# Kernel optimization log

Measured on AMD Instinct MI355X. Metric: run time of the kernel, lower is better.

The kernel has to match this reference:

```python
import jax, jax.numpy as jnp
import numpy as np

D_MODEL, D_INNER, D_STATE, DT_RANK, K = 768, 1536, 16, 48, 4
B, L = 2, 1024


def causal_depthwise_conv(x, w, b):
    # x: [B, L, D], w: [D, 1, K], b: [D]; torch pads K-1 both sides then slices [:L] -> causal left pad
    xt = x.transpose(0, 2, 1)  # [B, D, L]
    out = jax.lax.conv_general_dilated(
        xt, w, window_strides=(1,), padding=[(K - 1, 0)],
        dimension_numbers=('NCH', 'OIH', 'NCH'), feature_group_count=xt.shape[1])
    return out.transpose(0, 2, 1) + b


def ssm(xc, A_log, D, W_dt, dtW, dtb, W_B, W_C):
    # xc: [B, L, Din]
    A = -jnp.exp(A_log)                                   # [Din, N]
    dt_low = jnp.einsum('bld,rd->blr', xc, W_dt)          # [B, L, R]
    delta = jax.nn.softplus(jnp.einsum('blr,dr->bld', dt_low, dtW) + dtb)  # [B, L, Din]
    Bm = jnp.einsum('bld,nd->bln', xc, W_B)               # [B, L, N]
    Cm = jnp.einsum('bld,nd->bln', xc, W_C)               # [B, L, N]
    deltaA = jnp.exp(delta[..., None] * A)                # [B, L, Din, N]
    BX = (delta * xc)[..., None] * Bm[:, :, None, :]      # [B, L, Din, N]

    def combine(e1, e2):
        a1, b1 = e1
        a2, b2 = e2
        return a1 * a2, a2 * b1 + b2

    _, hs = jax.lax.associative_scan(combine, (deltaA, BX), axis=1)  # [B, L, Din, N]
    y = jnp.einsum('bldn,bln->bld', hs, Cm) + D * xc
    return y


def setup_inputs() -> dict:
    key = jax.random.key(0)
    ks = jax.random.split(key, 20)
    s = 0.02
    A_init = jnp.log(jnp.broadcast_to(jnp.arange(1, D_STATE + 1, dtype=jnp.float32), (D_INNER, D_STATE)))
    return {
        'x': jax.random.normal(ks[0], (B, L, D_MODEL), jnp.float32),
        'W_in_states': jax.random.normal(ks[1], (D_INNER, D_MODEL), jnp.float32) * s,
        'W_in_gates': jax.random.normal(ks[2], (D_INNER, D_MODEL), jnp.float32) * s,
        'conv_w': jax.random.normal(ks[3], (D_INNER, 1, K), jnp.float32) * 0.2,
        'conv_b': jax.random.normal(ks[4], (D_INNER,), jnp.float32) * 0.02,
        'conv_w_b': jax.random.normal(ks[5], (D_INNER, 1, K), jnp.float32) * 0.2,
        'conv_b_b': jax.random.normal(ks[6], (D_INNER,), jnp.float32) * 0.02,
        'W_dt': jax.random.normal(ks[7], (DT_RANK, D_INNER), jnp.float32) * s,
        'W_B': jax.random.normal(ks[8], (D_STATE, D_INNER), jnp.float32) * s,
        'W_C': jax.random.normal(ks[9], (D_STATE, D_INNER), jnp.float32) * s,
        'dtW': jax.random.normal(ks[10], (D_INNER, DT_RANK), jnp.float32) * s,
        'dtb': jax.random.normal(ks[11], (D_INNER,), jnp.float32) * 0.1,
        'A_log': A_init,
        'Dp': jnp.ones((D_INNER,), jnp.float32),
        'W_dt_b': jax.random.normal(ks[12], (DT_RANK, D_INNER), jnp.float32) * s,
        'W_B_b': jax.random.normal(ks[13], (D_STATE, D_INNER), jnp.float32) * s,
        'W_C_b': jax.random.normal(ks[14], (D_STATE, D_INNER), jnp.float32) * s,
        'dtW_b': jax.random.normal(ks[15], (D_INNER, DT_RANK), jnp.float32) * s,
        'dtb_b': jax.random.normal(ks[16], (D_INNER,), jnp.float32) * 0.1,
        'A_log_b': A_init,
        'Dp_b': jnp.ones((D_INNER,), jnp.float32),
        'W_out': jax.random.normal(ks[17], (D_MODEL, D_INNER), jnp.float32) * s,
    }


def reference(x, W_in_states, W_in_gates, conv_w, conv_b, conv_w_b, conv_b_b,
              W_dt, W_B, W_C, dtW, dtb, A_log, Dp,
              W_dt_b, W_B_b, W_C_b, dtW_b, dtb_b, A_log_b, Dp_b, W_out):
    xs = jnp.einsum('blm,dm->bld', x, W_in_states)  # [B, L, Din]
    z = jnp.einsum('blm,dm->bld', x, W_in_gates)    # [B, L, Din]
    # forward branch
    xc = jax.nn.silu(causal_depthwise_conv(xs, conv_w, conv_b))
    y = ssm(xc, A_log, Dp, W_dt, dtW, dtb, W_B, W_C)
    # backward branch: xz flipped along L, split -> reversed xs / reversed z
    xs_b = xs[:, ::-1]
    z_b = z[:, ::-1]
    xcb = jax.nn.silu(causal_depthwise_conv(xs_b, conv_w_b, conv_b_b))
    y_b = ssm(xcb, A_log_b, Dp_b, W_dt_b, dtW_b, dtb_b, W_B_b, W_C_b)
    # gating
    y = y * jax.nn.silu(z)
    y_b = y_b * jax.nn.silu(z_b)
    y = (y + y_b[:, ::-1]) * 0.5  # divide_output
    return jnp.einsum('bld,md->blm', y, W_out)
```

## Files before the change

kernel.cpp:

```cpp
#include <hip/hip_runtime.h>
#include <hip/hip_bf16.h>
#include <stdint.h>

#define DM 768
#define DI 1536
#define DSTATE 16
#define RNK 48
#define BB 2
#define LL 1024
#define ML (BB * LL)

#define NSEG 32
#define SEGL (LL / NSEG)

#define PROJ_NCHUNK 8
#define PROJ_KC (DI / PROJ_NCHUNK)

typedef unsigned short u16;
typedef __bf16 bf16x8 __attribute__((ext_vector_type(8)));
typedef float f32x4 __attribute__((ext_vector_type(4)));

struct __align__(8) u16x4_t { u16 x, y, z, w; };

__device__ __forceinline__ float b2f(u16 u) {
  union { uint32_t i; float f; } v; v.i = ((uint32_t)u) << 16; return v.f;
}
__device__ __forceinline__ u16 f2b(float f) {
  union { float f; uint32_t i; } v; v.f = f;
  uint32_t r = v.i + 0x7FFFu + ((v.i >> 16) & 1u);
  return (u16)(r >> 16);
}
__device__ __forceinline__ float silu_f(float x) { return x / (1.f + __expf(-x)); }
__device__ __forceinline__ float softplus_f(float s) {
  return fmaxf(s, 0.f) + __logf(1.f + __expf(-fabsf(s)));
}
__device__ __forceinline__ u16x4_t cvt4(float4 v) {
  u16x4_t o; o.x = f2b(v.x); o.y = f2b(v.y); o.z = f2b(v.z); o.w = f2b(v.w); return o;
}

__device__ __forceinline__ void gl16(const u16* g, u16* l) {
  __builtin_amdgcn_global_load_lds(
      (const __attribute__((address_space(1))) uint32_t*)g,
      (__attribute__((address_space(3))) uint32_t*)l, 16, 0, 0);
}

#define SEG_X    (ML * DM / 4)
#define SEG_W    (DI * DM / 4)
#define SEG_CAT  (128 * DI / 4)
#define SEG_DTW  (DI * 64 / 4)
__global__ __launch_bounds__(256) void convert_kernel(
    const float4* __restrict__ x, const float4* __restrict__ wis,
    const float4* __restrict__ wig, const float4* __restrict__ wout,
    const float* __restrict__ W_B, const float* __restrict__ W_C,
    const float* __restrict__ W_dt,
    const float* __restrict__ W_B_b, const float* __restrict__ W_C_b,
    const float* __restrict__ W_dt_b,
    const float* __restrict__ dtW, const float* __restrict__ dtW_b,
    u16x4_t* __restrict__ xb, u16x4_t* __restrict__ wisb,
    u16x4_t* __restrict__ wigb, u16x4_t* __restrict__ woutb,
    u16x4_t* __restrict__ wcf, u16x4_t* __restrict__ wcb,
    u16x4_t* __restrict__ dtwf, u16x4_t* __restrict__ dtwb)
{
  int idx = blockIdx.x * 256 + threadIdx.x;
  if (idx < SEG_X) { xb[idx] = cvt4(x[idx]); return; }
  idx -= SEG_X;
  if (idx < SEG_W) { wisb[idx] = cvt4(wis[idx]); return; }
  idx -= SEG_W;
  if (idx < SEG_W) { wigb[idx] = cvt4(wig[idx]); return; }
  idx -= SEG_W;
  if (idx < SEG_W) { woutb[idx] = cvt4(wout[idx]); return; }
  idx -= SEG_W;
  if (idx < 2 * SEG_CAT) {
    int dir = idx / SEG_CAT;
    int rem = idx % SEG_CAT;
    int row = rem / (DI / 4), k4 = rem % (DI / 4);
    const float* src = nullptr;
    if (row < 16)      src = (dir ? W_B_b  : W_B)  + (size_t)row * DI + k4 * 4;
    else if (row < 32) src = (dir ? W_C_b  : W_C)  + (size_t)(row - 16) * DI + k4 * 4;
    else if (row < 80) src = (dir ? W_dt_b : W_dt) + (size_t)(row - 32) * DI + k4 * 4;
    u16x4_t o;
    if (src) o = cvt4(*(const float4*)src);
    else { o.x = 0; o.y = 0; o.z = 0; o.w = 0; }
    (dir ? wcb : wcf)[rem] = o;
    return;
  }
  idx -= 2 * SEG_CAT;
  int dir = idx / SEG_DTW;
  int rem = idx % SEG_DTW;
  int d = rem / 16, r4 = rem % 16;
  const float* Dw = dir ? dtW_b : dtW;
  u16x4_t o;
  if (r4 < 12) o = cvt4(*(const float4*)(Dw + (size_t)d * RNK + r4 * 4));
  else { o.x = 0; o.y = 0; o.z = 0; o.w = 0; }
  (dir ? dtwb : dtwf)[rem] = o;
}

__global__ __launch_bounds__(256) void gemm_bt(
    const u16* __restrict__ A, const u16* __restrict__ B0,
    const u16* __restrict__ B1, int Nsplit,
    void* __restrict__ Cout, int M, int N, int K, int ldc, int epi,
    const u16* __restrict__ A2, const u16* __restrict__ B2,
    void* __restrict__ C2,
    const float* __restrict__ ebias, const float* __restrict__ ebias2)
{
  if (blockIdx.z) { A = A2; B0 = B2; Cout = C2; ebias = ebias2; }
  __shared__ alignas(16) u16 As[2][128 * 32];
  __shared__ alignas(16) u16 Bs[2][128 * 32];
  const int tid = threadIdx.x;
  const int wave = tid >> 6, lane = tid & 63;
  const int bm = blockIdx.y * 128;
  const int bn = blockIdx.x * 128;

  const u16* Bmat = B0;
  int ncol0 = bn;
  int epi_l = epi;
  if (B1 != nullptr && bn >= Nsplit) { Bmat = B1; ncol0 = bn - Nsplit; epi_l = 1; }

  const int c0 = tid, c1 = tid + 256;
  const u16* gA0 = A + (size_t)(bm + (c0 >> 2)) * K + (c0 & 3) * 8;
  const u16* gA1 = A + (size_t)(bm + (c1 >> 2)) * K + (c1 & 3) * 8;
  const u16* gB0 = Bmat + (size_t)(ncol0 + (c0 >> 2)) * K + (c0 & 3) * 8;
  const u16* gB1 = Bmat + (size_t)(ncol0 + (c1 >> 2)) * K + (c1 & 3) * 8;

  const int wm = (wave & 1) * 64, wn = (wave >> 1) * 64;
  const int rl = lane & 15, q = lane >> 4;

  f32x4 acc[4][4];
#pragma unroll
  for (int i = 0; i < 4; ++i)
#pragma unroll
    for (int j = 0; j < 4; ++j) acc[i][j] = (f32x4){0.f, 0.f, 0.f, 0.f};

  auto stage = [&](int buf, int k0) {
    gl16(gA0 + k0, &As[buf][c0 * 8]);
    gl16(gA1 + k0, &As[buf][c1 * 8]);
    gl16(gB0 + k0, &Bs[buf][c0 * 8]);
    gl16(gB1 + k0, &Bs[buf][c1 * 8]);
  };

  stage(0, 0);
  __syncthreads();
  int cur = 0;
  for (int k0 = 0; k0 < K; k0 += 32) {
    const bool more = (k0 + 32 < K);
    if (more) stage(cur ^ 1, k0 + 32);

    const bf16x8* AsV = (const bf16x8*)As[cur];
    const bf16x8* BsV = (const bf16x8*)Bs[cur];
    bf16x8 af[4], bfv[4];
#pragma unroll
    for (int s = 0; s < 4; ++s) {
      af[s]  = AsV[(wm + s * 16 + rl) * 4 + q];
      bfv[s] = BsV[(wn + s * 16 + rl) * 4 + q];
    }
#pragma unroll
    for (int i = 0; i < 4; ++i)
#pragma unroll
      for (int j = 0; j < 4; ++j)
        acc[i][j] = __builtin_amdgcn_mfma_f32_16x16x32_bf16(af[i], bfv[j], acc[i][j], 0, 0, 0);

    if (more) {
      __syncthreads();
      cur ^= 1;
    }
  }

#pragma unroll
  for (int i = 0; i < 4; ++i) {
#pragma unroll
    for (int j = 0; j < 4; ++j) {
#pragma unroll
      for (int r = 0; r < 4; ++r) {
        int row = bm + wm + i * 16 + q * 4 + r;
        int col = bn + wn + j * 16 + rl;
        float v = acc[i][j][r];
        if (epi_l == 1) v = silu_f(v);
        if (epi == 6) {
          ((u16*)Cout)[(size_t)row * ldc + col] = f2b(softplus_f(v + ebias[col]));
        } else {
          ((u16*)Cout)[(size_t)row * ldc + col] = f2b(v);
        }
      }
    }
  }
}

__global__ __launch_bounds__(256) void gemm_proj_sk(
    const u16* __restrict__ xcf, const u16* __restrict__ xcb,
    const u16* __restrict__ wcf, const u16* __restrict__ wcb,
    float* __restrict__ part)
{
  const int dir = blockIdx.z;
  const u16* A = dir ? xcb : xcf;
  const u16* B = dir ? wcb : wcf;
  const int kc = blockIdx.x;
  const int bm = blockIdx.y * 128;
  const int kbase = kc * PROJ_KC;

  __shared__ alignas(16) u16 As[128 * 32];
  __shared__ alignas(16) u16 Bs[128 * 32];
  const int tid = threadIdx.x;
  const int wave = tid >> 6, lane = tid & 63;
  const int c0 = tid, c1 = tid + 256;
  const u16* gA0 = A + (size_t)(bm + (c0 >> 2)) * DI + kbase + (c0 & 3) * 8;
  const u16* gA1 = A + (size_t)(bm + (c1 >> 2)) * DI + kbase + (c1 & 3) * 8;
  const u16* gB0 = B + (size_t)(c0 >> 2) * DI + kbase + (c0 & 3) * 8;
  const u16* gB1 = B + (size_t)(c1 >> 2) * DI + kbase + (c1 & 3) * 8;
  uint4* lA0 = (uint4*)&As[c0 * 8]; uint4* lA1 = (uint4*)&As[c1 * 8];
  uint4* lB0 = (uint4*)&Bs[c0 * 8]; uint4* lB1 = (uint4*)&Bs[c1 * 8];

  const int wm = (wave & 1) * 64, wn = (wave >> 1) * 64;
  const int rl = lane & 15, q = lane >> 4;

  f32x4 acc[4][4];
#pragma unroll
  for (int i = 0; i < 4; ++i)
#pragma unroll
    for (int j = 0; j < 4; ++j) acc[i][j] = (f32x4){0.f, 0.f, 0.f, 0.f};

  const bf16x8* AsV = (const bf16x8*)As;
  const bf16x8* BsV = (const bf16x8*)Bs;

  uint4 ra0 = *(const uint4*)(gA0);
  uint4 ra1 = *(const uint4*)(gA1);
  uint4 rb0 = *(const uint4*)(gB0);
  uint4 rb1 = *(const uint4*)(gB1);

  for (int k0 = 0; k0 < PROJ_KC; k0 += 32) {
    *lA0 = ra0; *lA1 = ra1; *lB0 = rb0; *lB1 = rb1;
    __syncthreads();
    if (k0 + 32 < PROJ_KC) {
      ra0 = *(const uint4*)(gA0 + k0 + 32);
      ra1 = *(const uint4*)(gA1 + k0 + 32);
      rb0 = *(const uint4*)(gB0 + k0 + 32);
      rb1 = *(const uint4*)(gB1 + k0 + 32);
    }
    bf16x8 af[4], bfv[4];
#pragma unroll
    for (int s = 0; s < 4; ++s) {
      af[s]  = AsV[(wm + s * 16 + rl) * 4 + q];
      bfv[s] = BsV[(wn + s * 16 + rl) * 4 + q];
    }
#pragma unroll
    for (int i = 0; i < 4; ++i)
#pragma unroll
      for (int j = 0; j < 4; ++j)
        acc[i][j] = __builtin_amdgcn_mfma_f32_16x16x32_bf16(af[i], bfv[j], acc[i][j], 0, 0, 0);
    __syncthreads();
  }

  float* pout = part + ((size_t)(dir * PROJ_NCHUNK + kc) * ML + bm) * 128;
#pragma unroll
  for (int i = 0; i < 4; ++i) {
#pragma unroll
    for (int j = 0; j < 4; ++j) {
#pragma unroll
      for (int r = 0; r < 4; ++r) {
        int row = wm + i * 16 + q * 4 + r;
        int col = wn + j * 16 + rl;
        if (col < 96)
          pout[(size_t)row * 128 + col] = acc[i][j][r];
      }
    }
  }
}

__global__ __launch_bounds__(256) void proj_reduce(
    const float* __restrict__ part,
    float* __restrict__ pf, float* __restrict__ pb,
    u16* __restrict__ dtlf, u16* __restrict__ dtlb)
{
  int idx = blockIdx.x * 256 + threadIdx.x;
  int col = idx % 96;
  int t = idx / 96;
  int row = t % ML;
  int dir = t / ML;
  const float* p = part + ((size_t)dir * PROJ_NCHUNK * ML + row) * 128 + col;
  float s = 0.f;
#pragma unroll
  for (int c = 0; c < PROJ_NCHUNK; ++c)
    s += p[(size_t)c * ML * 128];
  if (col < 32) (dir ? pb : pf)[(size_t)row * 32 + col] = s;
  else          (dir ? dtlb : dtlf)[(size_t)row * 64 + (col - 32)] = f2b(s);
}

__global__ __launch_bounds__(256) void gemm_out64(
    const u16* __restrict__ A, const u16* __restrict__ Bw,
    float* __restrict__ out)
{
  __shared__ alignas(16) u16 As[64 * 72];
  __shared__ alignas(16) u16 Bs[64 * 72];
  const int tid = threadIdx.x;
  const int wave = tid >> 6, lane = tid & 63;
  const int bm = blockIdx.y * 64;
  const int bn = blockIdx.x * 64;

  const int c0 = tid, c1 = tid + 256;
  const u16* gA0 = A + (size_t)(bm + (c0 >> 3)) * DI + (c0 & 7) * 8;
  const u16* gA1 = A + (size_t)(bm + (c1 >> 3)) * DI + (c1 & 7) * 8;
  const u16* gB0 = Bw + (size_t)(bn + (c0 >> 3)) * DI + (c0 & 7) * 8;
  const u16* gB1 = Bw + (size_t)(bn + (c1 >> 3)) * DI + (c1 & 7) * 8;
  uint4* lA0 = (uint4*)&As[(c0 >> 3) * 72 + (c0 & 7) * 8];
  uint4* lA1 = (uint4*)&As[(c1 >> 3) * 72 + (c1 & 7) * 8];
  uint4* lB0 = (uint4*)&Bs[(c0 >> 3) * 72 + (c0 & 7) * 8];
  uint4* lB1 = (uint4*)&Bs[(c1 >> 3) * 72 + (c1 & 7) * 8];

  const int rl = lane & 15, q = lane >> 4;

  f32x4 acc[4];
#pragma unroll
  for (int s = 0; s < 4; ++s) acc[s] = (f32x4){0.f, 0.f, 0.f, 0.f};

  uint4 ra0 = *(const uint4*)gA0, ra1 = *(const uint4*)gA1;
  uint4 rb0 = *(const uint4*)gB0, rb1 = *(const uint4*)gB1;

  for (int k0 = 0; k0 < DI; k0 += 64) {
    *lA0 = ra0; *lA1 = ra1; *lB0 = rb0; *lB1 = rb1;
    __syncthreads();
    if (k0 + 64 < DI) {
      ra0 = *(const uint4*)(gA0 + k0 + 64);
      ra1 = *(const uint4*)(gA1 + k0 + 64);
      rb0 = *(const uint4*)(gB0 + k0 + 64);
      rb1 = *(const uint4*)(gB1 + k0 + 64);
    }
    bf16x8 bf[2], af;
#pragma unroll
    for (int c = 0; c < 2; ++c)
      bf[c] = *(const bf16x8*)&Bs[(wave * 16 + rl) * 72 + c * 32 + q * 8];
#pragma unroll
    for (int s = 0; s < 4; ++s) {
#pragma unroll
      for (int c = 0; c < 2; ++c) {
        af = *(const bf16x8*)&As[(s * 16 + rl) * 72 + c * 32 + q * 8];
        acc[s] = __builtin_amdgcn_mfma_f32_16x16x32_bf16(af, bf[c], acc[s], 0, 0, 0);
      }
    }
    __syncthreads();
  }

#pragma unroll
  for (int s = 0; s < 4; ++s) {
#pragma unroll
    for (int r = 0; r < 4; ++r) {
      int row = bm + s * 16 + q * 4 + r;
      int col = bn + wave * 16 + rl;
      out[(size_t)row * DM + col] = acc[s][r];
    }
  }
}

__global__ void conv_kernel(
    const u16* __restrict__ xsg,
    const float* __restrict__ cw, const float* __restrict__ cb,
    const float* __restrict__ cwb, const float* __restrict__ cbb,
    u16* __restrict__ xc, u16* __restrict__ xcb)
{
  int idx = blockIdx.x * 256 + threadIdx.x;
  int d = idx % DI;
  int row = idx / DI;
  int l = row % LL, b = row / LL;
  const u16* base = xsg + (size_t)b * LL * 3072 + d;

  float4 wf = *(const float4*)(cw + d * 4);
  float4 wb = *(const float4*)(cwb + d * 4);
  float wfk[4] = {wf.x, wf.y, wf.z, wf.w};
  float wbk[4] = {wb.x, wb.y, wb.z, wb.w};

  float accf = cb[d];
  float accb = cbb[d];
#pragma unroll
  for (int k = 0; k < 4; ++k) {
    int ls = l - 3 + k;
    if (ls >= 0) {
      accf += wfk[k] * b2f(base[(size_t)ls * 3072]);
      accb += wbk[k] * b2f(base[(size_t)(LL - 1 - ls) * 3072]);
    }
  }
  xc[idx]  = f2b(silu_f(accf));
  xcb[idx] = f2b(silu_f(accb));
}

__global__ __launch_bounds__(256) void scan_sum(
    const u16* __restrict__ df, const u16* __restrict__ db,
    const u16* __restrict__ xcf, const u16* __restrict__ xcb,
    const float* __restrict__ pf, const float* __restrict__ pb,
    const float* __restrict__ A_log, const float* __restrict__ A_log_b,
    float* __restrict__ sdl, float* __restrict__ bs)
{
  const int dir = blockIdx.z / NSEG, seg = blockIdx.z % NSEG;
  const u16* delta = dir ? db : df;
  const u16* xc = dir ? xcb : xcf;
  const float* proj = dir ? pb : pf;
  const float* Al = dir ? A_log_b : A_log;
  const int b = blockIdx.y;
  const int d = blockIdx.x * 256 + threadIdx.x;
  const int l0 = seg * SEGL;

  __shared__ float Bsh[SEGL][16];
  for (int i = threadIdx.x; i < SEGL * 16; i += 256) {
    int l = i >> 4, n = i & 15;
    Bsh[l][n] = proj[((size_t)b * LL + l0 + l) * 32 + n];
  }
  __syncthreads();

  float An[16];
#pragma unroll
  for (int n = 0; n < 16; ++n) An[n] = -__expf(Al[d * 16 + n]);

  float h[16];
#pragma unroll
  for (int n = 0; n < 16; ++n) h[n] = 0.f;
  float S = 0.f;

  const u16* dbase = delta + ((size_t)b * LL + l0) * DI + d;
  const u16* xbase = xc + ((size_t)b * LL + l0) * DI + d;

  for (int g = 0; g < SEGL; g += 4) {
    float dl4[4], dx4[4];
#pragma unroll
    for (int j = 0; j < 4; ++j) {
      float dv = b2f(dbase[(size_t)(g + j) * DI]);
      float xv = b2f(xbase[(size_t)(g + j) * DI]);
      dl4[j] = dv; dx4[j] = dv * xv;
    }
#pragma unroll
    for (int j = 0; j < 4; ++j) {
      S += dl4[j];
#pragma unroll
      for (int n = 0; n < 16; ++n)
        h[n] = __expf(dl4[j] * An[n]) * h[n] + dx4[j] * Bsh[g + j][n];
    }
  }

  size_t base = (((size_t)dir * BB + b) * NSEG + seg) * DI + d;
  sdl[base] = S;
#pragma unroll
  for (int n = 0; n < 16; ++n) bs[base * 16 + n] = h[n];
}

__global__ __launch_bounds__(256) void scan_carry(
    const float* __restrict__ A_log, const float* __restrict__ A_log_b,
    const float* __restrict__ sdl, float* __restrict__ bs)
{
  int idx = blockIdx.x * 256 + threadIdx.x;
  int n = idx & 15;
  int t = idx >> 4;
  int d = t % DI;
  int b = (t / DI) % BB;
  int dir = t / (DI * BB);
  const float* Al = dir ? A_log_b : A_log;
  float An = -__expf(Al[d * 16 + n]);
  float h = 0.f;
  for (int s = 0; s < NSEG; ++s) {
    size_t base = (((size_t)dir * BB + b) * NSEG + s) * DI + d;
    float S = sdl[base];
    float bv = bs[base * 16 + n];
    bs[base * 16 + n] = h;
    h = __expf(S * An) * h + bv;
  }
}

__global__ __launch_bounds__(256) void scan_apply2(
    const u16* __restrict__ df, const u16* __restrict__ db,
    const u16* __restrict__ xcf, const u16* __restrict__ xcb,
    const float* __restrict__ pf, const float* __restrict__ pb,
    const float* __restrict__ A_log, const float* __restrict__ A_log_b,
    const float* __restrict__ Dp, const float* __restrict__ Dp_b,
    const float* __restrict__ bs, const u16* __restrict__ xsg,
    u16* __restrict__ yc)
{
  const int s = blockIdx.z;
  const int b = blockIdx.y;
  const int d = blockIdx.x * 256 + threadIdx.x;

  __shared__ float BCsh[SEGL][32];
  __shared__ u16 yfsh[SEGL][256];

  {
    const int l0 = s * SEGL;
    for (int i = threadIdx.x; i < SEGL * 32; i += 256) {
      int l = i >> 5, j = i & 31;
      BCsh[l][j] = pf[((size_t)b * LL + l0 + l) * 32 + j];
    }
    __syncthreads();

    float An[16];
#pragma unroll
    for (int n = 0; n < 16; ++n) An[n] = -__expf(A_log[d * 16 + n]);
    const float Dv = Dp[d];

    float h[16];
    size_t cbase = (((size_t)b) * NSEG + s) * DI + d;
#pragma unroll
    for (int n = 0; n < 16; ++n) h[n] = bs[cbase * 16 + n];

    const u16* dbase = df + ((size_t)b * LL + l0) * DI + d;
    const u16* xbase = xcf + ((size_t)b * LL + l0) * DI + d;

    for (int g = 0; g < SEGL; g += 4) {
      float dl4[4], xv4[4];
#pragma unroll
      for (int j = 0; j < 4; ++j) {
        dl4[j] = b2f(dbase[(size_t)(g + j) * DI]);
        xv4[j] = b2f(xbase[(size_t)(g + j) * DI]);
      }
#pragma unroll
      for (int j = 0; j < 4; ++j) {
        float dx = dl4[j] * xv4[j];
        float yv = 0.f;
#pragma unroll
        for (int n = 0; n < 16; ++n) {
          h[n] = __expf(dl4[j] * An[n]) * h[n] + dx * BCsh[g + j][n];
          yv += h[n] * BCsh[g + j][16 + n];
        }
        yfsh[g + j][threadIdx.x] = f2b(yv + Dv * xv4[j]);
      }
    }
    __syncthreads();
  }

  {
    const int seg1 = NSEG - 1 - s;
    const int l0r = seg1 * SEGL;
    for (int i = threadIdx.x; i < SEGL * 32; i += 256) {
      int l = i >> 5, j = i & 31;
      BCsh[l][j] = pb[((size_t)b * LL + l0r + l) * 32 + j];
    }
    __syncthreads();

    float An[16];
#pragma unroll
    for (int n = 0; n < 16; ++n) An[n] = -__expf(A_log_b[d * 16 + n]);
    const float Dv = Dp_b[d];

    float h[16];
    size_t cbase = (((size_t)BB + b) * NSEG + seg1) * DI + d;
#pragma unroll
    for (int n = 0; n < 16; ++n) h[n] = bs[cbase * 16 + n];

    const u16* dbase = db + ((size_t)b * LL + l0r) * DI + d;
    const u16* xbase = xcb + ((size_t)b * LL + l0r) * DI + d;

    for (int g = 0; g < SEGL; g += 4) {
      float dl4[4], xv4[4];
#pragma unroll
      for (int j = 0; j < 4; ++j) {
        dl4[j] = b2f(dbase[(size_t)(g + j) * DI]);
        xv4[j] = b2f(xbase[(size_t)(g + j) * DI]);
      }
#pragma unroll
      for (int j = 0; j < 4; ++j) {
        float dx = dl4[j] * xv4[j];
        float yv = 0.f;
#pragma unroll
        for (int n = 0; n < 16; ++n) {
          h[n] = __expf(dl4[j] * An[n]) * h[n] + dx * BCsh[g + j][n];
          yv += h[n] * BCsh[g + j][16 + n];
        }
        yv += Dv * xv4[j];
        int lrow = 31 - (g + j);
        int l = s * SEGL + lrow;
        float gate = b2f(xsg[((size_t)b * LL + l) * 3072 + DI + d]);
        float out = 0.5f * (b2f(yfsh[lrow][threadIdx.x]) + yv) * gate;
        yc[((size_t)b * LL + l) * DI + d] = f2b(out);
      }
    }
  }
}

extern "C" void kernel_launch(void* const* d_in, const int* in_sizes, int n_in,
                              void* d_out, int out_size, void* d_ws, size_t ws_size,
                              hipStream_t stream)
{
  const float* x       = (const float*)d_in[0];
  const float* Wis     = (const float*)d_in[1];
  const float* Wig     = (const float*)d_in[2];
  const float* conv_w  = (const float*)d_in[3];
  const float* conv_b  = (const float*)d_in[4];
  const float* conv_wb = (const float*)d_in[5];
  const float* conv_bb = (const float*)d_in[6];
  const float* W_dt    = (const float*)d_in[7];
  const float* W_B     = (const float*)d_in[8];
  const float* W_C     = (const float*)d_in[9];
  const float* dtW     = (const float*)d_in[10];
  const float* dtb     = (const float*)d_in[11];
  const float* A_log   = (const float*)d_in[12];
  const float* Dp      = (const float*)d_in[13];
  const float* W_dt_b  = (const float*)d_in[14];
  const float* W_B_b   = (const float*)d_in[15];
  const float* W_C_b   = (const float*)d_in[16];
  const float* dtW_b   = (const float*)d_in[17];
  const float* dtb_b   = (const float*)d_in[18];
  const float* A_log_b = (const float*)d_in[19];
  const float* Dp_b    = (const float*)d_in[20];
  const float* W_out   = (const float*)d_in[21];

  char* ws = (char*)d_ws;
  size_t off = 0;
  auto alloc = [&](size_t bytes) -> char* {
    char* p = ws + off; off += (bytes + 255) & ~(size_t)255; return p;
  };
  u16*   xb    = (u16*)alloc((size_t)ML * DM * 2);
  u16*   wisb  = (u16*)alloc((size_t)DI * DM * 2);
  u16*   wigb  = (u16*)alloc((size_t)DI * DM * 2);
  u16*   woutb = (u16*)alloc((size_t)DM * DI * 2);
  u16*   xsg = (u16*)alloc((size_t)ML * 3072 * 2);
  u16*   xc  = (u16*)alloc((size_t)ML * DI * 2);
  u16*   xcb = (u16*)alloc((size_t)ML * DI * 2);
  u16*   wcf = (u16*)alloc((size_t)128 * DI * 2);
  u16*   wcb = (u16*)alloc((size_t)128 * DI * 2);
  u16*   dtwf = (u16*)alloc((size_t)DI * 64 * 2);
  u16*   dtwb = (u16*)alloc((size_t)DI * 64 * 2);
  float* pf  = (float*)alloc((size_t)ML * 32 * 4);
  float* pb  = (float*)alloc((size_t)ML * 32 * 4);
  u16*   dtlf = (u16*)alloc((size_t)ML * 64 * 2);
  u16*   dtlb = (u16*)alloc((size_t)ML * 64 * 2);
  u16*   df  = (u16*)alloc((size_t)ML * DI * 2);
  u16*   db  = (u16*)alloc((size_t)ML * DI * 2);
  u16*   yc  = (u16*)alloc((size_t)ML * DI * 2);
  float* sdl = (float*)alloc((size_t)2 * BB * NSEG * DI * 4);
  float* bs  = (float*)alloc((size_t)2 * BB * NSEG * DI * 16 * 4);
  float* part = (float*)alloc((size_t)2 * PROJ_NCHUNK * ML * 128 * 4);

  const int conv_total = SEG_X + 3 * SEG_W + 2 * SEG_CAT + 2 * SEG_DTW;
  convert_kernel<<<(conv_total + 255) / 256, 256, 0, stream>>>(
      (const float4*)x, (const float4*)Wis, (const float4*)Wig, (const float4*)W_out,
      W_B, W_C, W_dt, W_B_b, W_C_b, W_dt_b, dtW, dtW_b,
      (u16x4_t*)xb, (u16x4_t*)wisb, (u16x4_t*)wigb, (u16x4_t*)woutb,
      (u16x4_t*)wcf, (u16x4_t*)wcb, (u16x4_t*)dtwf, (u16x4_t*)dtwb);

  gemm_bt<<<dim3(3072 / 128, ML / 128, 1), 256, 0, stream>>>(
      xb, wisb, wigb, DI, xsg, ML, 3072, DM, 3072, 0,
      nullptr, nullptr, nullptr, nullptr, nullptr);

  conv_kernel<<<(ML * DI) / 256, 256, 0, stream>>>(
      xsg, conv_w, conv_b, conv_wb, conv_bb, xc, xcb);

  gemm_proj_sk<<<dim3(PROJ_NCHUNK, ML / 128, 2), 256, 0, stream>>>(
      xc, xcb, wcf, wcb, part);
  proj_reduce<<<(2 * ML * 96) / 256, 256, 0, stream>>>(
      part, pf, pb, dtlf, dtlb);

  gemm_bt<<<dim3(DI / 128, ML / 128, 2), 256, 0, stream>>>(
      dtlf, dtwf, nullptr, 1 << 30, df, ML, DI, 64, DI, 6,
      dtlb, dtwb, db, dtb, dtb_b);

  scan_sum<<<dim3(DI / 256, BB, 2 * NSEG), 256, 0, stream>>>(
      df, db, xc, xcb, pf, pb, A_log, A_log_b, sdl, bs);
  scan_carry<<<(2 * BB * DI * 16) / 256, 256, 0, stream>>>(
      A_log, A_log_b, sdl, bs);
  scan_apply2<<<dim3(DI / 256, BB, NSEG), 256, 0, stream>>>(
      df, db, xc, xcb, pf, pb, A_log, A_log_b, Dp, Dp_b, bs, xsg, yc);

  gemm_out64<<<dim3(DM / 64, ML / 64, 1), 256, 0, stream>>>(
      yc, woutb, (float*)d_out);
}
```

Measured before the change: 269.4 us.

## Fuse split-K reduction into consumers and fold carry pass into scan apply

Drops the proj_reduce kernel. The split-K partial sums are now reduced inside a new dedicated delta GEMM (dt_low path) and inside the scan kernels when they load B/C into shared memory. It also drops the scan_carry kernel: each scan_apply block recomputes its incoming state by walking the prior segment summaries. This removes two launches and their intermediate buffers, at the cost of redundant partial-sum reads and a serial per-block carry loop whose length grows with the segment index.

```diff
diff --git a/kernel.cpp b/kernel.cpp
--- a/kernel.cpp
+++ b/kernel.cpp
@@ -98,12 +98,8 @@
 __global__ __launch_bounds__(256) void gemm_bt(
     const u16* __restrict__ A, const u16* __restrict__ B0,
     const u16* __restrict__ B1, int Nsplit,
-    void* __restrict__ Cout, int M, int N, int K, int ldc, int epi,
-    const u16* __restrict__ A2, const u16* __restrict__ B2,
-    void* __restrict__ C2,
-    const float* __restrict__ ebias, const float* __restrict__ ebias2)
-{
-  if (blockIdx.z) { A = A2; B0 = B2; Cout = C2; ebias = ebias2; }
+    void* __restrict__ Cout, int M, int N, int K, int ldc, int epi)
+{
   __shared__ alignas(16) u16 As[2][128 * 32];
   __shared__ alignas(16) u16 Bs[2][128 * 32];
   const int tid = threadIdx.x;
@@ -175,11 +171,7 @@
         int col = bn + wn + j * 16 + rl;
         float v = acc[i][j][r];
         if (epi_l == 1) v = silu_f(v);
-        if (epi == 6) {
-          ((u16*)Cout)[(size_t)row * ldc + col] = f2b(softplus_f(v + ebias[col]));
-        } else {
-          ((u16*)Cout)[(size_t)row * ldc + col] = f2b(v);
-        }
+        ((u16*)Cout)[(size_t)row * ldc + col] = f2b(v);
       }
     }
   }
@@ -265,23 +257,86 @@
   }
 }
 
-__global__ __launch_bounds__(256) void proj_reduce(
+__global__ __launch_bounds__(256) void gemm_delta(
     const float* __restrict__ part,
-    float* __restrict__ pf, float* __restrict__ pb,
-    u16* __restrict__ dtlf, u16* __restrict__ dtlb)
-{
-  int idx = blockIdx.x * 256 + threadIdx.x;
-  int col = idx % 96;
-  int t = idx / 96;
-  int row = t % ML;
-  int dir = t / ML;
-  const float* p = part + ((size_t)dir * PROJ_NCHUNK * ML + row) * 128 + col;
-  float s = 0.f;
-#pragma unroll
-  for (int c = 0; c < PROJ_NCHUNK; ++c)
-    s += p[(size_t)c * ML * 128];
-  if (col < 32) (dir ? pb : pf)[(size_t)row * 32 + col] = s;
-  else          (dir ? dtlb : dtlf)[(size_t)row * 64 + (col - 32)] = f2b(s);
+    const u16* __restrict__ dtwf, const u16* __restrict__ dtwb,
+    const float* __restrict__ dtb, const float* __restrict__ dtb_b,
+    u16* __restrict__ df, u16* __restrict__ db)
+{
+  const int dir = blockIdx.z;
+  const u16* Bw = dir ? dtwb : dtwf;
+  const float* eb = dir ? dtb_b : dtb;
+  u16* Cout = dir ? db : df;
+  const int bm = blockIdx.y * 128;
+  const int bn = blockIdx.x * 128;
+
+  __shared__ alignas(16) u16 As[128 * 64];
+  __shared__ alignas(16) u16 Bs[128 * 64];
+  const int tid = threadIdx.x;
+  const int wave = tid >> 6, lane = tid & 63;
+
+#pragma unroll
+  for (int i = 0; i < 4; ++i) {
+    int c = tid + i * 256;
+    gl16(Bw + (size_t)(bn + (c >> 3)) * 64 + (c & 7) * 8, &Bs[c * 8]);
+  }
+  const float* pb0 = part + (size_t)dir * PROJ_NCHUNK * ML * 128;
+#pragma unroll
+  for (int i = 0; i < 4; ++i) {
+    int c = tid + i * 256;
+    int row = c >> 3, kcol = (c & 7) * 8;
+    const float* p = pb0 + ((size_t)(bm + row)) * 128 + 32 + kcol;
+    float4 s0 = {0.f, 0.f, 0.f, 0.f}, s1 = {0.f, 0.f, 0.f, 0.f};
+#pragma unroll
+    for (int kc = 0; kc < PROJ_NCHUNK; ++kc) {
+      const float* pk = p + (size_t)kc * ML * 128;
+      float4 v0 = *(const float4*)pk;
+      float4 v1 = *(const float4*)(pk + 4);
+      s0.x += v0.x; s0.y += v0.y; s0.z += v0.z; s0.w += v0.w;
+      s1.x += v1.x; s1.y += v1.y; s1.z += v1.z; s1.w += v1.w;
+    }
+    u16 o[8] = {f2b(s0.x), f2b(s0.y), f2b(s0.z), f2b(s0.w),
+                f2b(s1.x), f2b(s1.y), f2b(s1.z), f2b(s1.w)};
+    *(uint4*)&As[c * 8] = *(const uint4*)o;
+  }
+  __syncthreads();
+
+  const int wm = (wave & 1) * 64, wn = (wave >> 1) * 64;
+  const int rl = lane & 15, q = lane >> 4;
+
+  f32x4 acc[4][4];
+#pragma unroll
+  for (int i = 0; i < 4; ++i)
+#pragma unroll
+    for (int j = 0; j < 4; ++j) acc[i][j] = (f32x4){0.f, 0.f, 0.f, 0.f};
+
+#pragma unroll
+  for (int kk = 0; kk < 2; ++kk) {
+    bf16x8 af[4], bfv[4];
+#pragma unroll
+    for (int s = 0; s < 4; ++s) {
+      af[s]  = *(const bf16x8*)&As[(wm + s * 16 + rl) * 64 + kk * 32 + q * 8];
+      bfv[s] = *(const bf16x8*)&Bs[(wn + s * 16 + rl) * 64 + kk * 32 + q * 8];
+    }
+#pragma unroll
+    for (int i = 0; i < 4; ++i)
+#pragma unroll
+      for (int j = 0; j < 4; ++j)
+        acc[i][j] = __builtin_amdgcn_mfma_f32_16x16x32_bf16(af[i], bfv[j], acc[i][j], 0, 0, 0);
+  }
+
+#pragma unroll
+  for (int i = 0; i < 4; ++i) {
+#pragma unroll
+    for (int j = 0; j < 4; ++j) {
+#pragma unroll
+      for (int r = 0; r < 4; ++r) {
+        int row = bm + wm + i * 16 + q * 4 + r;
+        int col = bn + wn + j * 16 + rl;
+        Cout[(size_t)row * DI + col] = f2b(softplus_f(acc[i][j][r] + eb[col]));
+      }
+    }
+  }
 }
 
 __global__ __launch_bounds__(256) void gemm_out64(
@@ -383,14 +438,14 @@
 __global__ __launch_bounds__(256) void scan_sum(
     const u16* __restrict__ df, const u16* __restrict__ db,
     const u16* __restrict__ xcf, const u16* __restrict__ xcb,
-    const float* __restrict__ pf, const float* __restrict__ pb,
+    const float* __restrict__ part,
     const float* __restrict__ A_log, const float* __restrict__ A_log_b,
     float* __restrict__ sdl, float* __restrict__ bs)
 {
   const int dir = blockIdx.z / NSEG, seg = blockIdx.z % NSEG;
   const u16* delta = dir ? db : df;
   const u16* xc = dir ? xcb : xcf;
-  const float* proj = dir ? pb : pf;
+  const float* pbase = part + (size_t)dir * PROJ_NCHUNK * ML * 128;
   const float* Al = dir ? A_log_b : A_log;
   const int b = blockIdx.y;
   const int d = blockIdx.x * 256 + threadIdx.x;
@@ -399,7 +454,11 @@
   __shared__ float Bsh[SEGL][16];
   for (int i = threadIdx.x; i < SEGL * 16; i += 256) {
     int l = i >> 4, n = i & 15;
-    Bsh[l][n] = proj[((size_t)b * LL + l0 + l) * 32 + n];
+    const float* p = pbase + ((size_t)(b * LL + l0 + l)) * 128 + n;
+    float s = 0.f;
+#pragma unroll
+    for (int kc = 0; kc < PROJ_NCHUNK; ++kc) s += p[(size_t)kc * ML * 128];
+    Bsh[l][n] = s;
   }
   __syncthreads();
 
@@ -438,36 +497,14 @@
   for (int n = 0; n < 16; ++n) bs[base * 16 + n] = h[n];
 }
 
-__global__ __launch_bounds__(256) void scan_carry(
-    const float* __restrict__ A_log, const float* __restrict__ A_log_b,
-    const float* __restrict__ sdl, float* __restrict__ bs)
-{
-  int idx = blockIdx.x * 256 + threadIdx.x;
-  int n = idx & 15;
-  int t = idx >> 4;
-  int d = t % DI;
-  int b = (t / DI) % BB;
-  int dir = t / (DI * BB);
-  const float* Al = dir ? A_log_b : A_log;
-  float An = -__expf(Al[d * 16 + n]);
-  float h = 0.f;
-  for (int s = 0; s < NSEG; ++s) {
-    size_t base = (((size_t)dir * BB + b) * NSEG + s) * DI + d;
-    float S = sdl[base];
-    float bv = bs[base * 16 + n];
-    bs[base * 16 + n] = h;
-    h = __expf(S * An) * h + bv;
-  }
-}
-
 __global__ __launch_bounds__(256) void scan_apply2(
     const u16* __restrict__ df, const u16* __restrict__ db,
     const u16* __restrict__ xcf, const u16* __restrict__ xcb,
-    const float* __restrict__ pf, const float* __restrict__ pb,
+    const float* __restrict__ part,
     const float* __restrict__ A_log, const float* __restrict__ A_log_b,
     const float* __restrict__ Dp, const float* __restrict__ Dp_b,
-    const float* __restrict__ bs, const u16* __restrict__ xsg,
-    u16* __restrict__ yc)
+    const float* __restrict__ sdl, const float* __restrict__ bs,
+    const u16* __restrict__ xsg, u16* __restrict__ yc)
 {
   const int s = blockIdx.z;
   const int b = blockIdx.y;
@@ -480,7 +517,11 @@
     const int l0 = s * SEGL;
     for (int i = threadIdx.x; i < SEGL * 32; i += 256) {
       int l = i >> 5, j = i & 31;
-      BCsh[l][j] = pf[((size_t)b * LL + l0 + l) * 32 + j];
+      const float* p = part + ((size_t)(b * LL + l0 + l)) * 128 + j;
+      float sum = 0.f;
+#pragma unroll
+      for (int kc = 0; kc < PROJ_NCHUNK; ++kc) sum += p[(size_t)kc * ML * 128];
+      BCsh[l][j] = sum;
     }
     __syncthreads();
 
@@ -490,9 +531,15 @@
     const float Dv = Dp[d];
 
     float h[16];
-    size_t cbase = (((size_t)b) * NSEG + s) * DI + d;
-#pragma unroll
-    for (int n = 0; n < 16; ++n) h[n] = bs[cbase * 16 + n];
+#pragma unroll
+    for (int n = 0; n < 16; ++n) h[n] = 0.f;
+    for (int t = 0; t < s; ++t) {
+      size_t cb = (((size_t)b) * NSEG + t) * DI + d;
+      float S = sdl[cb];
+#pragma unroll
+      for (int n = 0; n < 16; ++n)
+        h[n] = __expf(S * An[n]) * h[n] + bs[cb * 16 + n];
+    }
 
     const u16* dbase = df + ((size_t)b * LL + l0) * DI + d;
     const u16* xbase = xcf + ((size_t)b * LL + l0) * DI + d;
@@ -522,9 +569,14 @@
   {
     const int seg1 = NSEG - 1 - s;
     const int l0r = seg1 * SEGL;
+    const float* pbase1 = part + (size_t)PROJ_NCHUNK * ML * 128;
     for (int i = threadIdx.x; i < SEGL * 32; i += 256) {
       int l = i >> 5, j = i & 31;
-      BCsh[l][j] = pb[((size_t)b * LL + l0r + l) * 32 + j];
+      const float* p = pbase1 + ((size_t)(b * LL + l0r + l)) * 128 + j;
+      float sum = 0.f;
+#pragma unroll
+      for (int kc = 0; kc < PROJ_NCHUNK; ++kc) sum += p[(size_t)kc * ML * 128];
+      BCsh[l][j] = sum;
     }
     __syncthreads();
 
@@ -534,9 +586,15 @@
     const float Dv = Dp_b[d];
 
     float h[16];
-    size_t cbase = (((size_t)BB + b) * NSEG + seg1) * DI + d;
-#pragma unroll
-    for (int n = 0; n < 16; ++n) h[n] = bs[cbase * 16 + n];
+#pragma unroll
+    for (int n = 0; n < 16; ++n) h[n] = 0.f;
+    for (int t = 0; t < seg1; ++t) {
+      size_t cb = (((size_t)BB + b) * NSEG + t) * DI + d;
+      float S = sdl[cb];
+#pragma unroll
+      for (int n = 0; n < 16; ++n)
+        h[n] = __expf(S * An[n]) * h[n] + bs[cb * 16 + n];
+    }
 
     const u16* dbase = db + ((size_t)b * LL + l0r) * DI + d;
     const u16* xbase = xcb + ((size_t)b * LL + l0r) * DI + d;
@@ -611,10 +669,6 @@
   u16*   wcb = (u16*)alloc((size_t)128 * DI * 2);
   u16*   dtwf = (u16*)alloc((size_t)DI * 64 * 2);
   u16*   dtwb = (u16*)alloc((size_t)DI * 64 * 2);
-  float* pf  = (float*)alloc((size_t)ML * 32 * 4);
-  float* pb  = (float*)alloc((size_t)ML * 32 * 4);
-  u16*   dtlf = (u16*)alloc((size_t)ML * 64 * 2);
-  u16*   dtlb = (u16*)alloc((size_t)ML * 64 * 2);
   u16*   df  = (u16*)alloc((size_t)ML * DI * 2);
   u16*   db  = (u16*)alloc((size_t)ML * DI * 2);
   u16*   yc  = (u16*)alloc((size_t)ML * DI * 2);
@@ -630,27 +684,21 @@
       (u16x4_t*)wcf, (u16x4_t*)wcb, (u16x4_t*)dtwf, (u16x4_t*)dtwb);
 
   gemm_bt<<<dim3(3072 / 128, ML / 128, 1), 256, 0, stream>>>(
-      xb, wisb, wigb, DI, xsg, ML, 3072, DM, 3072, 0,
-      nullptr, nullptr, nullptr, nullptr, nullptr);
+      xb, wisb, wigb, DI, xsg, ML, 3072, DM, 3072, 0);
 
   conv_kernel<<<(ML * DI) / 256, 256, 0, stream>>>(
       xsg, conv_w, conv_b, conv_wb, conv_bb, xc, xcb);
 
   gemm_proj_sk<<<dim3(PROJ_NCHUNK, ML / 128, 2), 256, 0, stream>>>(
       xc, xcb, wcf, wcb, part);
-  proj_reduce<<<(2 * ML * 96) / 256, 256, 0, stream>>>(
-      part, pf, pb, dtlf, dtlb);
-
-  gemm_bt<<<dim3(DI / 128, ML / 128, 2), 256, 0, stream>>>(
-      dtlf, dtwf, nullptr, 1 << 30, df, ML, DI, 64, DI, 6,
-      dtlb, dtwb, db, dtb, dtb_b);
+
+  gemm_delta<<<dim3(DI / 128, ML / 128, 2), 256, 0, stream>>>(
+      part, dtwf, dtwb, dtb, dtb_b, df, db);
 
   scan_sum<<<dim3(DI / 256, BB, 2 * NSEG), 256, 0, stream>>>(
-      df, db, xc, xcb, pf, pb, A_log, A_log_b, sdl, bs);
-  scan_carry<<<(2 * BB * DI * 16) / 256, 256, 0, stream>>>(
-      A_log, A_log_b, sdl, bs);
+      df, db, xc, xcb, part, A_log, A_log_b, sdl, bs);
   scan_apply2<<<dim3(DI / 256, BB, NSEG), 256, 0, stream>>>(
-      df, db, xc, xcb, pf, pb, A_log, A_log_b, Dp, Dp_b, bs, xsg, yc);
+      df, db, xc, xcb, part, A_log, A_log_b, Dp, Dp_b, sdl, bs, xsg, yc);
 
   gemm_out64<<<dim3(DM / 64, ML / 64, 1), 256, 0, stream>>>(
       yc, woutb, (float*)d_out);
```

New measurement: 274.2 us. Within noise of the previous version (+1.8%).

## Run forward and backward scan directions concurrently in scan_apply2; add dedicated delta GEMM

Applied to the files above, without the earlier changes.

scan_apply2 now launches 512 threads per block, with each half running one direction's segment scan at the same time instead of one after the other. Both results are staged in shared memory and a cooperative pass combines them with the gate. The delta projection moves from the generic double-buffered gemm_bt to a specialised gemm_delta kernel that loads the full K=64 tile in one go, and gemm_bt loses its blockIdx.z / epilogue branches. The aim is to halve the serial recurrence latency per block and cut GEMM overhead, at the cost of more registers and shared memory per block, which can lower occupancy.

```diff
diff --git a/kernel.cpp b/kernel.cpp
--- a/kernel.cpp
+++ b/kernel.cpp
@@ -98,12 +98,8 @@
 __global__ __launch_bounds__(256) void gemm_bt(
     const u16* __restrict__ A, const u16* __restrict__ B0,
     const u16* __restrict__ B1, int Nsplit,
-    void* __restrict__ Cout, int M, int N, int K, int ldc, int epi,
-    const u16* __restrict__ A2, const u16* __restrict__ B2,
-    void* __restrict__ C2,
-    const float* __restrict__ ebias, const float* __restrict__ ebias2)
-{
-  if (blockIdx.z) { A = A2; B0 = B2; Cout = C2; ebias = ebias2; }
+    void* __restrict__ Cout, int M, int N, int K, int ldc, int epi)
+{
   __shared__ alignas(16) u16 As[2][128 * 32];
   __shared__ alignas(16) u16 Bs[2][128 * 32];
   const int tid = threadIdx.x;
@@ -175,11 +171,7 @@
         int col = bn + wn + j * 16 + rl;
         float v = acc[i][j][r];
         if (epi_l == 1) v = silu_f(v);
-        if (epi == 6) {
-          ((u16*)Cout)[(size_t)row * ldc + col] = f2b(softplus_f(v + ebias[col]));
-        } else {
-          ((u16*)Cout)[(size_t)row * ldc + col] = f2b(v);
-        }
+        ((u16*)Cout)[(size_t)row * ldc + col] = f2b(v);
       }
     }
   }
@@ -282,6 +274,71 @@
     s += p[(size_t)c * ML * 128];
   if (col < 32) (dir ? pb : pf)[(size_t)row * 32 + col] = s;
   else          (dir ? dtlb : dtlf)[(size_t)row * 64 + (col - 32)] = f2b(s);
+}
+
+__global__ __launch_bounds__(256) void gemm_delta(
+    const u16* __restrict__ dtlf, const u16* __restrict__ dtlb,
+    const u16* __restrict__ dtwf, const u16* __restrict__ dtwb,
+    const float* __restrict__ dtb, const float* __restrict__ dtb_b,
+    u16* __restrict__ df, u16* __restrict__ db)
+{
+  const int dir = blockIdx.z;
+  const u16* A = dir ? dtlb : dtlf;
+  const u16* Bw = dir ? dtwb : dtwf;
+  const float* eb = dir ? dtb_b : dtb;
+  u16* Cout = dir ? db : df;
+  const int bm = blockIdx.y * 128;
+  const int bn = blockIdx.x * 128;
+
+  __shared__ alignas(16) u16 As[128 * 64];
+  __shared__ alignas(16) u16 Bs[128 * 64];
+  const int tid = threadIdx.x;
+  const int wave = tid >> 6, lane = tid & 63;
+
+#pragma unroll
+  for (int i = 0; i < 4; ++i) {
+    int c = tid + i * 256;
+    gl16(A  + (size_t)(bm + (c >> 3)) * 64 + (c & 7) * 8, &As[c * 8]);
+    gl16(Bw + (size_t)(bn + (c >> 3)) * 64 + (c & 7) * 8, &Bs[c * 8]);
+  }
+  __syncthreads();
+
+  const int wm = (wave & 1) * 64, wn = (wave >> 1) * 64;
+  const int rl = lane & 15, q = lane >> 4;
+
+  f32x4 acc[4][4];
+#pragma unroll
+  for (int i = 0; i < 4; ++i)
+#pragma unroll
+    for (int j = 0; j < 4; ++j) acc[i][j] = (f32x4){0.f, 0.f, 0.f, 0.f};
+
+#pragma unroll
+  for (int kk = 0; kk < 2; ++kk) {
+    bf16x8 af[4], bfv[4];
+#pragma unroll
+    for (int s = 0; s < 4; ++s) {
+      af[s]  = *(const bf16x8*)&As[(wm + s * 16 + rl) * 64 + kk * 32 + q * 8];
+      bfv[s] = *(const bf16x8*)&Bs[(wn + s * 16 + rl) * 64 + kk * 32 + q * 8];
+    }
+#pragma unroll
+    for (int i = 0; i < 4; ++i)
+#pragma unroll
+      for (int j = 0; j < 4; ++j)
+        acc[i][j] = __builtin_amdgcn_mfma_f32_16x16x32_bf16(af[i], bfv[j], acc[i][j], 0, 0, 0);
+  }
+
+#pragma unroll
+  for (int i = 0; i < 4; ++i) {
+#pragma unroll
+    for (int j = 0; j < 4; ++j) {
+#pragma unroll
+      for (int r = 0; r < 4; ++r) {
+        int row = bm + wm + i * 16 + q * 4 + r;
+        int col = bn + wn + j * 16 + rl;
+        Cout[(size_t)row * DI + col] = f2b(softplus_f(acc[i][j][r] + eb[col]));
+      }
+    }
+  }
 }
 
 __global__ __launch_bounds__(256) void gemm_out64(
@@ -460,7 +517,7 @@
   }
 }
 
-__global__ __launch_bounds__(256) void scan_apply2(
+__global__ __launch_bounds__(512) void scan_apply2(
     const u16* __restrict__ df, const u16* __restrict__ db,
     const u16* __restrict__ xcf, const u16* __restrict__ xcb,
     const float* __restrict__ pf, const float* __restrict__ pb,
@@ -471,100 +528,70 @@
 {
   const int s = blockIdx.z;
   const int b = blockIdx.y;
-  const int d = blockIdx.x * 256 + threadIdx.x;
-
-  __shared__ float BCsh[SEGL][32];
-  __shared__ u16 yfsh[SEGL][256];
-
-  {
-    const int l0 = s * SEGL;
-    for (int i = threadIdx.x; i < SEGL * 32; i += 256) {
-      int l = i >> 5, j = i & 31;
-      BCsh[l][j] = pf[((size_t)b * LL + l0 + l) * 32 + j];
-    }
-    __syncthreads();
-
-    float An[16];
-#pragma unroll
-    for (int n = 0; n < 16; ++n) An[n] = -__expf(A_log[d * 16 + n]);
-    const float Dv = Dp[d];
-
-    float h[16];
-    size_t cbase = (((size_t)b) * NSEG + s) * DI + d;
-#pragma unroll
-    for (int n = 0; n < 16; ++n) h[n] = bs[cbase * 16 + n];
-
-    const u16* dbase = df + ((size_t)b * LL + l0) * DI + d;
-    const u16* xbase = xcf + ((size_t)b * LL + l0) * DI + d;
-
-    for (int g = 0; g < SEGL; g += 4) {
-      float dl4[4], xv4[4];
-#pragma unroll
-      for (int j = 0; j < 4; ++j) {
-        dl4[j] = b2f(dbase[(size_t)(g + j) * DI]);
-        xv4[j] = b2f(xbase[(size_t)(g + j) * DI]);
+  const int tid = threadIdx.x;
+  const int half = tid >> 8;
+  const int td = tid & 255;
+  const int d = blockIdx.x * 256 + td;
+
+  __shared__ float BCsh[2][SEGL][32];
+  __shared__ u16 ysh[2][SEGL][256];
+
+  const int seg = half ? (NSEG - 1 - s) : s;
+  const int l0 = seg * SEGL;
+  const float* proj = half ? pb : pf;
+  const float* Al   = half ? A_log_b : A_log;
+  const float* Dpp  = half ? Dp_b : Dp;
+  const u16* delta  = half ? db : df;
+  const u16* xc     = half ? xcb : xcf;
+
+  for (int i = td; i < SEGL * 32; i += 256) {
+    int l = i >> 5, j = i & 31;
+    BCsh[half][l][j] = proj[((size_t)b * LL + l0 + l) * 32 + j];
+  }
+  __syncthreads();
+
+  float An[16];
+#pragma unroll
+  for (int n = 0; n < 16; ++n) An[n] = -__expf(Al[d * 16 + n]);
+  const float Dv = Dpp[d];
+
+  float h[16];
+  size_t cbase = (((size_t)half * BB + b) * NSEG + seg) * DI + d;
+#pragma unroll
+  for (int n = 0; n < 16; ++n) h[n] = bs[cbase * 16 + n];
+
+  const u16* dbase = delta + ((size_t)b * LL + l0) * DI + d;
+  const u16* xbase = xc + ((size_t)b * LL + l0) * DI + d;
+
+  for (int g = 0; g < SEGL; g += 4) {
+    float dl4[4], xv4[4];
+#pragma unroll
+    for (int j = 0; j < 4; ++j) {
+      dl4[j] = b2f(dbase[(size_t)(g + j) * DI]);
+      xv4[j] = b2f(xbase[(size_t)(g + j) * DI]);
+    }
+#pragma unroll
+    for (int j = 0; j < 4; ++j) {
+      float dx = dl4[j] * xv4[j];
+      float yv = 0.f;
+#pragma unroll
+      for (int n = 0; n < 16; ++n) {
+        h[n] = __expf(dl4[j] * An[n]) * h[n] + dx * BCsh[half][g + j][n];
+        yv += h[n] * BCsh[half][g + j][16 + n];
       }
-#pragma unroll
-      for (int j = 0; j < 4; ++j) {
-        float dx = dl4[j] * xv4[j];
-        float yv = 0.f;
-#pragma unroll
-        for (int n = 0; n < 16; ++n) {
-          h[n] = __expf(dl4[j] * An[n]) * h[n] + dx * BCsh[g + j][n];
-          yv += h[n] * BCsh[g + j][16 + n];
-        }
-        yfsh[g + j][threadIdx.x] = f2b(yv + Dv * xv4[j]);
-      }
-    }
-    __syncthreads();
-  }
-
-  {
-    const int seg1 = NSEG - 1 - s;
-    const int l0r = seg1 * SEGL;
-    for (int i = threadIdx.x; i < SEGL * 32; i += 256) {
-      int l = i >> 5, j = i & 31;
-      BCsh[l][j] = pb[((size_t)b * LL + l0r + l) * 32 + j];
-    }
-    __syncthreads();
-
-    float An[16];
-#pragma unroll
-    for (int n = 0; n < 16; ++n) An[n] = -__expf(A_log_b[d * 16 + n]);
-    const float Dv = Dp_b[d];
-
-    float h[16];
-    size_t cbase = (((size_t)BB + b) * NSEG + seg1) * DI + d;
-#pragma unroll
-    for (int n = 0; n < 16; ++n) h[n] = bs[cbase * 16 + n];
-
-    const u16* dbase = db + ((size_t)b * LL + l0r) * DI + d;
-    const u16* xbase = xcb + ((size_t)b * LL + l0r) * DI + d;
-
-    for (int g = 0; g < SEGL; g += 4) {
-      float dl4[4], xv4[4];
-#pragma unroll
-      for (int j = 0; j < 4; ++j) {
-        dl4[j] = b2f(dbase[(size_t)(g + j) * DI]);
-        xv4[j] = b2f(xbase[(size_t)(g + j) * DI]);
-      }
-#pragma unroll
-      for (int j = 0; j < 4; ++j) {
-        float dx = dl4[j] * xv4[j];
-        float yv = 0.f;
-#pragma unroll
-        for (int n = 0; n < 16; ++n) {
-          h[n] = __expf(dl4[j] * An[n]) * h[n] + dx * BCsh[g + j][n];
-          yv += h[n] * BCsh[g + j][16 + n];
-        }
-        yv += Dv * xv4[j];
-        int lrow = 31 - (g + j);
-        int l = s * SEGL + lrow;
-        float gate = b2f(xsg[((size_t)b * LL + l) * 3072 + DI + d]);
-        float out = 0.5f * (b2f(yfsh[lrow][threadIdx.x]) + yv) * gate;
-        yc[((size_t)b * LL + l) * DI + d] = f2b(out);
-      }
-    }
+      ysh[half][g + j][td] = f2b(yv + Dv * xv4[j]);
+    }
+  }
+  __syncthreads();
+
+  for (int i = tid; i < SEGL * 256; i += 512) {
+    int lrow = i >> 8, dd = i & 255;
+    int l = s * SEGL + lrow;
+    int dg = blockIdx.x * 256 + dd;
+    float gate = b2f(xsg[((size_t)b * LL + l) * 3072 + DI + dg]);
+    float out = 0.5f * (b2f(ysh[0][lrow][dd]) +
+                        b2f(ysh[1][SEGL - 1 - lrow][dd])) * gate;
+    yc[((size_t)b * LL + l) * DI + dg] = f2b(out);
   }
 }
 
@@ -630,8 +657,7 @@
       (u16x4_t*)wcf, (u16x4_t*)wcb, (u16x4_t*)dtwf, (u16x4_t*)dtwb);
 
   gemm_bt<<<dim3(3072 / 128, ML / 128, 1), 256, 0, stream>>>(
-      xb, wisb, wigb, DI, xsg, ML, 3072, DM, 3072, 0,
-      nullptr, nullptr, nullptr, nullptr, nullptr);
+      xb, wisb, wigb, DI, xsg, ML, 3072, DM, 3072, 0);
 
   conv_kernel<<<(ML * DI) / 256, 256, 0, stream>>>(
       xsg, conv_w, conv_b, conv_wb, conv_bb, xc, xcb);
@@ -641,15 +667,14 @@
   proj_reduce<<<(2 * ML * 96) / 256, 256, 0, stream>>>(
       part, pf, pb, dtlf, dtlb);
 
-  gemm_bt<<<dim3(DI / 128, ML / 128, 2), 256, 0, stream>>>(
-      dtlf, dtwf, nullptr, 1 << 30, df, ML, DI, 64, DI, 6,
-      dtlb, dtwb, db, dtb, dtb_b);
+  gemm_delta<<<dim3(DI / 128, ML / 128, 2), 256, 0, stream>>>(
+      dtlf, dtlb, dtwf, dtwb, dtb, dtb_b, df, db);
 
   scan_sum<<<dim3(DI / 256, BB, 2 * NSEG), 256, 0, stream>>>(
       df, db, xc, xcb, pf, pb, A_log, A_log_b, sdl, bs);
   scan_carry<<<(2 * BB * DI * 16) / 256, 256, 0, stream>>>(
       A_log, A_log_b, sdl, bs);
-  scan_apply2<<<dim3(DI / 256, BB, NSEG), 256, 0, stream>>>(
+  scan_apply2<<<dim3(DI / 256, BB, NSEG), 512, 0, stream>>>(
       df, db, xc, xcb, pf, pb, A_log, A_log_b, Dp, Dp_b, bs, xsg, yc);
 
   gemm_out64<<<dim3(DM / 64, ML / 64, 1), 256, 0, stream>>>(
```

Measured after the change: 258.0 us. 4.2% less time.
